# Kernel tuning notes

Measured on AMD Instinct MI355X. Metric: run time of the kernel, lower is better.

Reference implementation:

```python
import jax, jax.numpy as jnp
import numpy as np

B, NH, T, H, W = 2, 4, 8, 14, 14
DIM = 384
HD = DIM // NH  # 96 = head_dim = depthwise conv channels
N = T * H * W  # 1568 tokens, no cls
EPS = 1e-6


def _dwconv3d(x, w):
    # x: [BN, C, T, H, W], w: [C, 1, 3, 3, 3]; depthwise conv, stride 1, pad 1
    return jax.lax.conv_general_dilated(
        x, w, window_strides=(1, 1, 1), padding=[(1, 1)] * 3,
        feature_group_count=x.shape[1],
        dimension_numbers=('NCDHW', 'OIDHW', 'NCDHW'))


def _layernorm(x, g, b):
    m = jnp.mean(x, axis=-1, keepdims=True)
    v = jnp.var(x, axis=-1, keepdims=True)
    return (x - m) * jax.lax.rsqrt(v + EPS) * g + b


def _attention_pool(x4, conv_w, ln_g, ln_b, t, h, w):
    # x4: [B, nh, L, c] with L = t*h*w (no cls token)
    Bq, n, L, c = x4.shape
    y = x4.reshape(Bq * n, t, h, w, c).transpose(0, 4, 1, 2, 3)  # [(b nh), c, t, h, w]
    y = _dwconv3d(y, conv_w)
    y = y.transpose(0, 2, 3, 4, 1).reshape(Bq, n, L, c)
    return _layernorm(y, ln_g, ln_b)


def setup_inputs() -> dict:
    key = jax.random.key(0)
    ks = jax.random.split(key, 12)
    inp = {
        'x': jax.random.normal(ks[0], (B, N, DIM), jnp.float32),
        'qkv_w': jax.random.normal(ks[1], (3 * DIM, DIM), jnp.float32) * 0.02,
        'proj_w': jax.random.normal(ks[2], (DIM, DIM), jnp.float32) * 0.02,
        'proj_b': jnp.zeros((DIM,), jnp.float32),
        'pool_q_w': jax.random.normal(ks[3], (HD, 1, 3, 3, 3), jnp.float32) * 0.1,
        'pool_k_w': jax.random.normal(ks[4], (HD, 1, 3, 3, 3), jnp.float32) * 0.1,
        'pool_v_w': jax.random.normal(ks[5], (HD, 1, 3, 3, 3), jnp.float32) * 0.1,
        'norm_q_w': jnp.ones((HD,), jnp.float32), 'norm_q_b': jnp.zeros((HD,), jnp.float32),
        'norm_k_w': jnp.ones((HD,), jnp.float32), 'norm_k_b': jnp.zeros((HD,), jnp.float32),
        'norm_v_w': jnp.ones((HD,), jnp.float32), 'norm_v_b': jnp.zeros((HD,), jnp.float32),
        'rel_pos_h': jax.random.normal(ks[6], (2 * H - 1, HD), jnp.float32) * 0.02,
        'rel_pos_w': jax.random.normal(ks[7], (2 * W - 1, HD), jnp.float32) * 0.02,
        'rel_pos_t': jax.random.normal(ks[8], (2 * T - 1, HD), jnp.float32) * 0.02,
        't': T, 'h': H, 'w': W,
    }
    return inp


def reference(x, qkv_w, proj_w, proj_b, pool_q_w, pool_k_w, pool_v_w,
              norm_q_w, norm_q_b, norm_k_w, norm_k_b, norm_v_w, norm_v_b,
              rel_pos_h, rel_pos_w, rel_pos_t, t, h, w):
    Bq, Nq, _ = x.shape
    # fused QKV projection (qkv_bias=False)
    qkv = (x @ qkv_w.T).reshape(Bq, Nq, 3, NH, HD).transpose(2, 0, 3, 1, 4)
    q, k, v = qkv[0], qkv[1], qkv[2]  # [B, nh, N, hd]
    # pooled Q/K/V: depthwise conv3d + LayerNorm (stride 1 -> shapes preserved)
    q = _attention_pool(q, pool_q_w, norm_q_w, norm_q_b, t, h, w)
    k = _attention_pool(k, pool_k_w, norm_k_w, norm_k_b, t, h, w)
    v = _attention_pool(v, pool_v_w, norm_v_w, norm_v_b, t, h, w)

    scale = HD ** -0.5
    attn = jnp.einsum('bnqc,bnkc->bnqk', q * scale, k)  # [B, nh, N, N]

    # decomposed relative position biases (q_shape == k_shape, ratios == 1)
    dist_h = jnp.arange(h)[:, None] - jnp.arange(h)[None, :] + (h - 1)
    dist_w = jnp.arange(w)[:, None] - jnp.arange(w)[None, :] + (w - 1)
    dist_t = jnp.arange(t)[:, None] - jnp.arange(t)[None, :] + (t - 1)
    Rh = rel_pos_h[dist_h]  # [h, h, c]
    Rw = rel_pos_w[dist_w]  # [w, w, c]
    Rt = rel_pos_t[dist_t]  # [t, t, c]

    r_q = q.reshape(Bq, NH, t, h, w, HD)
    rel_h = jnp.einsum('bnthwc,hkc->bnthwk', r_q, Rh)  # [B,nh,t,h,w,kh]
    rel_w = jnp.einsum('bnthwc,wkc->bnthwk', r_q, Rw)  # [B,nh,t,h,w,kw]
    rel_t = jnp.einsum('bnthwc,tkc->bnthwk', r_q, Rt)  # [B,nh,t,h,w,kt]

    attn8 = attn.reshape(Bq, NH, t, h, w, t, h, w)
    attn8 = (attn8
             + rel_h[:, :, :, :, :, None, :, None]
             + rel_w[:, :, :, :, :, None, None, :]
             + rel_t[:, :, :, :, :, :, None, None])
    attn = jax.nn.softmax(attn8.reshape(Bq, NH, Nq, Nq), axis=-1)

    out = jnp.einsum('bnqk,bnkc->bnqc', attn, v)
    out = out + q  # residual pooling
    out = out.transpose(0, 2, 1, 3).reshape(Bq, Nq, DIM)
    out = out @ proj_w.T + proj_b
    return out
```

## Files before the change

kernel.cpp:

```cpp
#include <hip/hip_runtime.h>

#define B_    2
#define NH_   4
#define T_    8
#define H_    14
#define W_    14
#define HW_   196
#define HD_   96
#define DIM_  384
#define N_    1568
#define BH_   (B_*NH_)
#define BN_   (B_*N_)
#define BHN_  (BH_*N_)
#define CAUG_ 160

typedef unsigned short bf_t;
typedef unsigned int   u32;
typedef __attribute__((ext_vector_type(8))) short bf16x8;
typedef __attribute__((ext_vector_type(4))) float f32x4;

#define LOG2E 1.4426950408889634f
#define QSCALE_LOG2E 0.14724445f

static __device__ __forceinline__ float lo16(u32 v){ union{u32 i; float f;}x; x.i = v<<16;           return x.f; }
static __device__ __forceinline__ float hi16(u32 v){ union{u32 i; float f;}x; x.i = v & 0xffff0000u; return x.f; }
static __device__ __forceinline__ float b2f(bf_t v){ union{u32 i; float f;}x; x.i = ((u32)v)<<16;    return x.f; }
static __device__ __forceinline__ bf_t  f2b(float f){
  union{float f; u32 i;} x; x.f = f;
  return (bf_t)((x.i + 0x7fffu + ((x.i>>16)&1u)) >> 16);
}
static __device__ __forceinline__ u32 pack2(float a, float b){
  return (u32)f2b(a) | ((u32)f2b(b) << 16);
}
static __device__ __forceinline__ size_t ftidx(int row, int k){
  return ((((size_t)(row>>4))*12 + (k>>5))*64 + ((k>>3)&3)*16 + (row&15))*8 + (k&7);
}

#define NA_ (BN_*DIM_)
#define NB_ (3*DIM_*DIM_)
#define NC_ (DIM_*DIM_)
#define CAST_BLOCKS ((NA_+NB_+NC_)/4/256)

__global__ __launch_bounds__(256) void k_cast(
    const float* __restrict__ a, bf_t* __restrict__ ad,
    const float* __restrict__ b, bf_t* __restrict__ bd,
    const float* __restrict__ c, bf_t* __restrict__ cd,
    const float* __restrict__ wq, const float* __restrict__ wk,
    const float* __restrict__ wv, float* __restrict__ tq,
    float* __restrict__ tk, float* __restrict__ tv){
  if (blockIdx.x < CAST_BLOCKS){
    const int i = blockIdx.x*256 + threadIdx.x;
    const int i4 = i*4;
    float4 v; bf_t* dst; int row, k;
    if (i4 < NA_){
      v = ((const float4*)a)[i];
      dst = ad; row = i4/DIM_; k = i4%DIM_;
    } else if (i4 < NA_+NB_){
      const int f = i4 - NA_;
      v = ((const float4*)b)[i - NA_/4];
      dst = bd; row = f/DIM_; k = f%DIM_;
    } else {
      const int f = i4 - NA_ - NB_;
      v = ((const float4*)c)[i - (NA_+NB_)/4];
      dst = cd; row = f/DIM_; k = f%DIM_;
    }
    ushort4 o; o.x = f2b(v.x); o.y = f2b(v.y); o.z = f2b(v.z); o.w = f2b(v.w);
    *(ushort4*)(dst + ftidx(row, k)) = o;
  } else {
    const int idx = (blockIdx.x - CAST_BLOCKS)*256 + threadIdx.x;
    if (idx >= 3*HD_*27) return;
    const int t = idx / (HD_*27), rem = idx % (HD_*27);
    const int ch = rem / 27, j = rem % 27;
    const float* s = (t==0)? wq : (t==1)? wk : wv;
    float* d       = (t==0)? tq : (t==1)? tk : tv;
    d[j*HD_ + ch] = s[ch*27 + j];
  }
}

__global__ __launch_bounds__(256) void k_qkv(const bf_t* __restrict__ Xt,
    const bf_t* __restrict__ Wt,
    bf_t* __restrict__ q, bf_t* __restrict__ k, bf_t* __restrict__ v){
  const int wid = threadIdx.x >> 6, lane = threadIdx.x & 63;
  const int wr = wid & 1, wc = wid >> 1;
  const int nl = lane & 15, quad = lane >> 4;
  const int r0 = blockIdx.x*64 + wr*32;
  const int mt0 = r0 >> 4;
  const int nt0 = blockIdx.y*8 + wc*4;
  f32x4 acc[2][4];
  #pragma unroll
  for (int i = 0; i < 2; ++i)
    #pragma unroll
    for (int j = 0; j < 4; ++j) acc[i][j] = (f32x4){0.f,0.f,0.f,0.f};
  const bf_t* A0 = Xt + ((size_t)mt0*12*64 + lane)*8;
  const bf_t* B0 = Wt + ((size_t)nt0*12*64 + lane)*8;
  #pragma unroll 2
  for (int k0 = 0; k0 < 12; ++k0){
    const bf16x8 a0 = *(const bf16x8*)(A0 + k0*512);
    const bf16x8 a1 = *(const bf16x8*)(A0 + 12*512 + k0*512);
    bf16x8 bf[4];
    #pragma unroll
    for (int j = 0; j < 4; ++j) bf[j] = *(const bf16x8*)(B0 + (size_t)(j*12 + k0)*512);
    #pragma unroll
    for (int j = 0; j < 4; ++j){
      acc[0][j] = __builtin_amdgcn_mfma_f32_16x16x32_bf16(a0, bf[j], acc[0][j], 0, 0, 0);
      acc[1][j] = __builtin_amdgcn_mfma_f32_16x16x32_bf16(a1, bf[j], acc[1][j], 0, 0, 0);
    }
  }
  #pragma unroll
  for (int i = 0; i < 2; ++i){
    #pragma unroll
    for (int r = 0; r < 4; ++r){
      const int m  = r0 + i*16 + quad*4 + r;
      const int bb = m / N_, nn = m % N_;
      #pragma unroll
      for (int j = 0; j < 4; ++j){
        const int col = (nt0 + j)*16 + nl;
        const int s = col / DIM_, rem = col - s*DIM_;
        const int head = rem / HD_, hc = rem % HD_;
        bf_t* dst = (s==0) ? q : (s==1) ? k : v;
        dst[((size_t)(bb*NH_ + head)*N_ + nn)*HD_ + hc] = f2b(acc[i][j][r]);
      }
    }
  }
}

static __device__ __forceinline__ void ln_butterfly(
    float v0, float v1, float& mean, float& rstd){
  float s  = v0 + v1;
  float s2 = v0*v0 + v1*v1;
  #pragma unroll
  for (int off = 32; off > 0; off >>= 1){
    s  += __shfl_xor(s,  off);
    s2 += __shfl_xor(s2, off);
  }
  mean = s * (1.f/HD_);
  const float var = fmaxf(s2*(1.f/HD_) - mean*mean, 0.f);
  rstd = rsqrtf(var + 1e-6f);
}

__global__ __launch_bounds__(256) void k_pool_slab(
    const bf_t* __restrict__ qr_, const bf_t* __restrict__ kr_, const bf_t* __restrict__ vr_,
    const float* __restrict__ wtq, const float* __restrict__ wtk, const float* __restrict__ wtv,
    const float* __restrict__ gq, const float* __restrict__ bq,
    const float* __restrict__ gk, const float* __restrict__ bk,
    const float* __restrict__ gv, const float* __restrict__ bv,
    const float* __restrict__ rph, const float* __restrict__ rpw,
    const float* __restrict__ rpt,
    bf_t* __restrict__ qp, bf_t* __restrict__ Qaug,
    bf_t* __restrict__ Kt, bf_t* __restrict__ Vtt){
  __shared__ __align__(16) bf_t slab[162][HD_];
  __shared__ float qtmp[4][4][HD_];
  __shared__ u32 vres[16][48];
  const int wid = threadIdx.x >> 6, lane = threadIdx.x & 63;
  const int sec = blockIdx.x / 784;
  const int rr_ = blockIdx.x % 784;
  const int bh = rr_ / 98, tok0 = (rr_ % 98)*16;
  const bf_t*  src = (sec==0)? qr_ : (sec==1)? kr_ : vr_;
  const float* wt  = (sec==0)? wtq : (sec==1)? wtk : wtv;
  const float* g   = (sec==0)? gq  : (sec==1)? gk  : gv;
  const float* be  = (sec==0)? bq  : (sec==1)? bk  : bv;
  const bf_t* base = src + (size_t)bh*N_*HD_;

  for (int li = threadIdx.x; li < 162*12; li += 256){
    const int rw = li / 12, ss = li % 12;
    const int aa = rw/54, bb2 = (rw%54)/18, cc = rw%18;
    int nn = tok0 + (aa-1)*HW_ + (bb2-1)*W_ + (cc-1);
    nn = min(max(nn, 0), N_-1);
    *(uint4*)&slab[rw][ss*8] = *(const uint4*)(base + (size_t)nn*HD_ + ss*8);
  }
  __syncthreads();

  const int c0 = (lane < 48) ? 2*lane : 0;
  float2 wgt[27];
  #pragma unroll
  for (int j = 0; j < 27; ++j) wgt[j] = *(const float2*)(wt + j*HD_ + c0);
  const float gg0 = g[c0], gg1 = g[c0+1], be0 = be[c0], be1 = be[c0+1];

  #pragma unroll 1
  for (int tk = 0; tk < 4; ++tk){
    const int u = wid*4 + tk;
    const int n = tok0 + u;
    const int tt = n / HW_; const int rm = n % HW_;
    const int hh = rm / W_, ww = rm % W_;
    float v0 = 0.f, v1 = 0.f;
    #pragma unroll
    for (int j = 0; j < 27; ++j){
      const int dt = j/9 - 1, dh = (j%9)/3 - 1, dw = j%3 - 1;
      const bool ok = ((unsigned)(tt+dt) < (unsigned)T_)
                   && ((unsigned)(hh+dh) < (unsigned)H_)
                   && ((unsigned)(ww+dw) < (unsigned)W_);
      const int rj = (dt+1)*54 + (dh+1)*18 + (dw + u + 1);
      u32 d = *(const u32*)&slab[rj][c0];
      d = ok ? d : 0u;
      v0 = fmaf(wgt[j].x, lo16(d), v0);
      v1 = fmaf(wgt[j].y, hi16(d), v1);
    }
    if (lane >= 48){ v0 = 0.f; v1 = 0.f; }
    float mean, rstd;
    ln_butterfly(v0, v1, mean, rstd);
    const float y0 = (v0 - mean)*rstd*gg0 + be0;
    const float y1 = (v1 - mean)*rstd*gg1 + be1;

    if (sec == 0){
      const int token = bh*N_ + n;
      if (lane < 48){
        ((u32*)qp)  [(size_t)token*48 + lane] = pack2(y0, y1);
        ((u32*)Qaug)[(size_t)token*80 + lane] = pack2(y0*QSCALE_LOG2E, y1*QSCALE_LOG2E);
        qtmp[wid][tk][c0] = y0; qtmp[wid][tk][c0+1] = y1;
      }
      __syncthreads();
      if (lane < 36){
        const float* tb; int idx;
        if (lane < 14)      { tb = rph; idx = hh - lane      + 13; }
        else if (lane < 28) { tb = rpw; idx = ww - (lane-14) + 13; }
        else                { tb = rpt; idx = tt - (lane-28) +  7; }
        const float4* t4 = (const float4*)(tb + (size_t)idx*HD_);
        float acc = 0.f;
        #pragma unroll
        for (int i = 0; i < 24; ++i){
          const float4 rv = t4[i];
          acc += qtmp[wid][tk][4*i]*rv.x + qtmp[wid][tk][4*i+1]*rv.y
               + qtmp[wid][tk][4*i+2]*rv.z + qtmp[wid][tk][4*i+3]*rv.w;
        }
        Qaug[(size_t)token*CAUG_ + HD_ + lane] = f2b(acc * LOG2E);
      } else if (lane < 64){
        Qaug[(size_t)token*CAUG_ + HD_ + lane] = 0;
      }
    } else if (sec == 1){
      const int tl = n >> 4, nr = n & 15;
      if (lane < 48){
        const size_t idx = ((((size_t)bh*98 + tl)*5 + (lane>>4))*64
                           + ((lane&15)>>2)*16 + nr)*4 + (lane&3);
        ((u32*)Kt)[idx] = pack2(y0, y1);
      } else {
        const int m = lane - 48;
        u32 pr_[2];
        #pragma unroll
        for (int h2 = 0; h2 < 2; ++h2){
          u32 w_ = 0;
          #pragma unroll
          for (int e = 0; e < 2; ++e){
            const int jj = 4*m + 2*h2 + e;
            bool on = (jj < 14) ? (jj == hh) : (jj < 28) ? (jj-14 == ww)
                     : (jj < 36) ? (jj-28 == tt) : false;
            if (on) w_ |= (0x3F80u << (16*e));
          }
          pr_[h2] = w_;
        }
        const size_t bidx = ((((size_t)bh*98 + tl)*5 + (3 + (m>>3)))*64
                            + ((m&7)>>1)*16 + nr)*4 + 2*(m&1);
        *(uint2*)((u32*)Kt + bidx) = make_uint2(pr_[0], pr_[1]);
      }
    } else {
      if (lane < 48) vres[u][lane] = pack2(y0, y1);
    }
  }

  if (sec == 2){
    __syncthreads();
    if (threadIdx.x < 2*HD_){
      const int grp = threadIdx.x / HD_, c = threadIdx.x % HD_;
      const int t0g = grp*8;
      u32 o[4];
      #pragma unroll
      for (int i = 0; i < 4; ++i){
        const u32 a = vres[t0g + 2*i][c>>1], b = vres[t0g + 2*i+1][c>>1];
        const u32 ra = (c&1) ? (a >> 16) : (a & 0xffffu);
        const u32 rb = (c&1) ? (b >> 16) : (b & 0xffffu);
        o[i] = ra | (rb << 16);
      }
      const int n0g = tok0 + t0g;
      const int pr = n0g >> 5, qd = (n0g & 31) >> 3;
      bf_t* dst = Vtt + ((((size_t)bh*49 + pr)*6 + (c>>4))*64 + qd*16 + (c&15))*8;
      *(uint4*)dst = make_uint4(o[0], o[1], o[2], o[3]);
    }
  }
}

__global__ __launch_bounds__(512) void k_attn(
    const bf_t* __restrict__ Qaug, const bf_t* __restrict__ Kt,
    const bf_t* __restrict__ Vtt, const bf_t* __restrict__ qp,
    bf_t* __restrict__ attb){
  __shared__ __align__(16) short Pb[8][16][40];
  __shared__ bf_t Os[8][16][96];
  __shared__ float ms[8][16], ls[8][16];
  const int wid = threadIdx.x >> 6, lane = threadIdx.x & 63;
  const int bh = blockIdx.x / 98, qt = blockIdx.x % 98;
  const int q0 = qt*16;
  const int nl = lane & 15, quad = lane >> 4;

  bf16x8 qa[5];
  {
    const bf_t* Qrow = Qaug + ((size_t)bh*N_ + q0 + nl)*CAUG_ + quad*8;
    #pragma unroll
    for (int i = 0; i < 5; ++i) qa[i] = *(const bf16x8*)(Qrow + i*32);
  }
  short* Pw = &Pb[wid][0][0];

  f32x4 O[6];
  #pragma unroll
  for (int i = 0; i < 6; ++i) O[i] = (f32x4){0.f,0.f,0.f,0.f};
  float mc[4]   = {0.f,0.f,0.f,0.f};
  float rmax[4] = {-3e38f,-3e38f,-3e38f,-3e38f};
  float l[4]    = {0.f,0.f,0.f,0.f};

  auto s_tile = [&](int tl, int half){
    const bf_t* Kp = Kt + (((size_t)bh*98 + tl)*5*64 + lane)*8;
    f32x4 s = (f32x4){0.f,0.f,0.f,0.f};
    #pragma unroll
    for (int i = 0; i < 5; ++i)
      s = __builtin_amdgcn_mfma_f32_16x16x32_bf16(qa[i], *(const bf16x8*)(Kp + i*512), s, 0, 0, 0);
    #pragma unroll
    for (int r = 0; r < 4; ++r){
      rmax[r] = fmaxf(rmax[r], s[r]);
      const float p = exp2f(s[r] - mc[r]);
      l[r] += p;
      Pw[(quad*4 + r)*40 + half*16 + nl] = (short)f2b(p);
    }
  };
  auto rescale = [&](){
    #pragma unroll
    for (int r = 0; r < 4; ++r){
      float tm = rmax[r];
      tm = fmaxf(tm, __shfl_xor(tm, 1));
      tm = fmaxf(tm, __shfl_xor(tm, 2));
      tm = fmaxf(tm, __shfl_xor(tm, 4));
      tm = fmaxf(tm, __shfl_xor(tm, 8));
      const float mn = fmaxf(mc[r], tm);
      const float al = exp2f(mc[r] - mn);
      mc[r] = mn; l[r] *= al;
      #pragma unroll
      for (int ct = 0; ct < 6; ++ct) O[ct][r] *= al;
    }
  };

  const int p0 = (wid == 0) ? 0 : (7 + 6*(wid-1));
  const int npairs = (wid == 0) ? 7 : 6;
  #pragma unroll 1
  for (int pi = 0; pi < npairs; ++pi){
    const int kp = p0 + pi;
    s_tile(2*kp,     0);
    s_tile(2*kp + 1, 1);
    const bf16x8 pa = *(const bf16x8*)(Pw + nl*40 + quad*8);
    const bf_t* Vp = Vtt + (((size_t)bh*49 + kp)*6*64 + lane)*8;
    #pragma unroll
    for (int ct = 0; ct < 6; ++ct)
      O[ct] = __builtin_amdgcn_mfma_f32_16x16x32_bf16(pa, *(const bf16x8*)(Vp + ct*512), O[ct], 0, 0, 0);
    if (pi == npairs-1) rescale();
  }

  #pragma unroll
  for (int r = 0; r < 4; ++r){
    float ls_ = l[r];
    ls_ += __shfl_xor(ls_, 1); ls_ += __shfl_xor(ls_, 2);
    ls_ += __shfl_xor(ls_, 4); ls_ += __shfl_xor(ls_, 8);
    if (nl == 0){ ms[wid][quad*4 + r] = mc[r]; ls[wid][quad*4 + r] = ls_; }
    #pragma unroll
    for (int ct = 0; ct < 6; ++ct) Os[wid][quad*4 + r][ct*16 + nl] = f2b(O[ct][r]);
  }
  __syncthreads();

  const int bb = bh >> 2, head = bh & 3;
  const int grow0 = bb*N_ + q0;
  for (int e = threadIdx.x; e < 16*96; e += 512){
    const int row = e / 96, col = e % 96;
    float mx = -3e38f;
    #pragma unroll
    for (int w = 0; w < 8; ++w) mx = fmaxf(mx, ms[w][row]);
    float L = 0.f, A = 0.f;
    #pragma unroll
    for (int w = 0; w < 8; ++w){
      const float wt = exp2f(ms[w][row] - mx);
      L += wt*ls[w][row];
      A += wt*b2f(Os[w][row][col]);
    }
    const float val = A/L + b2f(qp[((size_t)bh*N_ + q0 + row)*HD_ + col]);
    attb[ftidx(grow0 + row, head*HD_ + col)] = f2b(val);
  }
}

__global__ __launch_bounds__(256) void k_proj(const bf_t* __restrict__ At,
    const bf_t* __restrict__ Wpt, const float* __restrict__ pb,
    float* __restrict__ out){
  const int wid = threadIdx.x >> 6, lane = threadIdx.x & 63;
  const int wr = wid & 1, wc = wid >> 1;
  const int nl = lane & 15, quad = lane >> 4;
  const int r0 = blockIdx.x*64 + wr*32;
  const int mt0 = r0 >> 4;
  const int nt0 = blockIdx.y*8 + wc*4;
  f32x4 acc[2][4];
  #pragma unroll
  for (int i = 0; i < 2; ++i)
    #pragma unroll
    for (int j = 0; j < 4; ++j) acc[i][j] = (f32x4){0.f,0.f,0.f,0.f};
  const bf_t* A0 = At  + ((size_t)mt0*12*64 + lane)*8;
  const bf_t* B0 = Wpt + ((size_t)nt0*12*64 + lane)*8;
  #pragma unroll 2
  for (int k0 = 0; k0 < 12; ++k0){
    const bf16x8 a0 = *(const bf16x8*)(A0 + k0*512);
    const bf16x8 a1 = *(const bf16x8*)(A0 + 12*512 + k0*512);
    bf16x8 bf[4];
    #pragma unroll
    for (int j = 0; j < 4; ++j) bf[j] = *(const bf16x8*)(B0 + (size_t)(j*12 + k0)*512);
    #pragma unroll
    for (int j = 0; j < 4; ++j){
      acc[0][j] = __builtin_amdgcn_mfma_f32_16x16x32_bf16(a0, bf[j], acc[0][j], 0, 0, 0);
      acc[1][j] = __builtin_amdgcn_mfma_f32_16x16x32_bf16(a1, bf[j], acc[1][j], 0, 0, 0);
    }
  }
  #pragma unroll
  for (int i = 0; i < 2; ++i){
    #pragma unroll
    for (int r = 0; r < 4; ++r){
      const int m = r0 + i*16 + quad*4 + r;
      #pragma unroll
      for (int j = 0; j < 4; ++j){
        const int col = (nt0 + j)*16 + nl;
        out[(size_t)m*DIM_ + col] = acc[i][j][r] + pb[col];
      }
    }
  }
}

extern "C" void kernel_launch(void* const* d_in, const int* in_sizes, int n_in,
                              void* d_out, int out_size, void* d_ws, size_t ws_size,
                              hipStream_t stream){
  const float* x      = (const float*)d_in[0];
  const float* qkv_w  = (const float*)d_in[1];
  const float* proj_w = (const float*)d_in[2];
  const float* proj_b = (const float*)d_in[3];
  const float* pqw    = (const float*)d_in[4];
  const float* pkw    = (const float*)d_in[5];
  const float* pvw    = (const float*)d_in[6];
  const float* nqw    = (const float*)d_in[7];
  const float* nqb    = (const float*)d_in[8];
  const float* nkw    = (const float*)d_in[9];
  const float* nkb    = (const float*)d_in[10];
  const float* nvw    = (const float*)d_in[11];
  const float* nvb    = (const float*)d_in[12];
  const float* rph    = (const float*)d_in[13];
  const float* rpw    = (const float*)d_in[14];
  const float* rpt    = (const float*)d_in[15];

  char* p = (char*)d_ws;
  const size_t RAW = (size_t)BH_*N_*HD_*2;
  const size_t AUG = (size_t)BH_*N_*CAUG_*2;
  bf_t* xb     = (bf_t*)(p);
  bf_t* wqkvb  = (bf_t*)(p + RAW);
  bf_t* wprojb = (bf_t*)(p + RAW + 884736);
  char* p2 = p + RAW + 884736 + 294912;
  bf_t* raw_q  = (bf_t*)(p2);
  bf_t* raw_k  = (bf_t*)(p2 + RAW);
  bf_t* raw_v  = (bf_t*)(p2 + 2*RAW);
  bf_t* attb   = raw_q;
  bf_t* qp     = (bf_t*)(p2 + 3*RAW);
  bf_t* Qaug   = (bf_t*)(p2 + 4*RAW);
  bf_t* Kt     = (bf_t*)(p2 + 4*RAW + AUG);
  bf_t* Vtt    = (bf_t*)(p2 + 4*RAW + 2*AUG);
  float* wtq   = (float*)(p2 + 4*RAW + 2*AUG + RAW);
  float* wtk   = wtq + 27*HD_;
  float* wtv   = wtk + 27*HD_;

  k_cast     <<<CAST_BLOCKS + 31, 256, 0, stream>>>(x, xb, qkv_w, wqkvb, proj_w, wprojb,
                                                    pqw, pkw, pvw, wtq, wtk, wtv);
  k_qkv      <<<dim3(BN_/64, 9),  256, 0, stream>>>(xb, wqkvb, raw_q, raw_k, raw_v);
  k_pool_slab<<<3*784,            256, 0, stream>>>(raw_q, raw_k, raw_v,
                                                    wtq, wtk, wtv,
                                                    nqw, nqb, nkw, nkb, nvw, nvb,
                                                    rph, rpw, rpt,
                                                    qp, Qaug, Kt, Vtt);
  k_attn     <<<BH_*98,           512, 0, stream>>>(Qaug, Kt, Vtt, qp, attb);
  k_proj     <<<dim3(BN_/64, 3),  256, 0, stream>>>(attb, wprojb, proj_b, (float*)d_out);
}
```

Baseline: 202.5 us.

## Reuse slab rows across four tokens and alias pool kernel shared memory

The depthwise conv in the pool kernel now loads six consecutive slab rows per (dt,dh) offset and reuses them across the four tokens each wave handles. Before, each token re-read its own 27 neighbours. Shared buffers for slab, qtmp and vres are merged into a union to cut LDS footprint, and the launch bounds request 5 blocks per CU for higher occupancy. The weight loads are hoisted ahead of the slab fill so they overlap it. Barriers are added to protect the aliased storage, and register pressure rises because four accumulators are live at once.

```diff
diff --git a/kernel.cpp b/kernel.cpp
--- a/kernel.cpp
+++ b/kernel.cpp
@@ -138,7 +138,13 @@
   rstd = rsqrtf(var + 1e-6f);
 }
 
-__global__ __launch_bounds__(256) void k_pool_slab(
+union PoolSM {
+  bf_t  slab[162][HD_];
+  float qtmp[4][4][HD_];
+  u32   vres[16][48];
+};
+
+__global__ __launch_bounds__(256, 5) void k_pool_slab(
     const bf_t* __restrict__ qr_, const bf_t* __restrict__ kr_, const bf_t* __restrict__ vr_,
     const float* __restrict__ wtq, const float* __restrict__ wtk, const float* __restrict__ wtv,
     const float* __restrict__ gq, const float* __restrict__ bq,
@@ -148,9 +154,7 @@
     const float* __restrict__ rpt,
     bf_t* __restrict__ qp, bf_t* __restrict__ Qaug,
     bf_t* __restrict__ Kt, bf_t* __restrict__ Vtt){
-  __shared__ __align__(16) bf_t slab[162][HD_];
-  __shared__ float qtmp[4][4][HD_];
-  __shared__ u32 vres[16][48];
+  __shared__ __align__(16) PoolSM sm;
   const int wid = threadIdx.x >> 6, lane = threadIdx.x & 63;
   const int sec = blockIdx.x / 784;
   const int rr_ = blockIdx.x % 784;
@@ -161,77 +165,106 @@
   const float* be  = (sec==0)? bq  : (sec==1)? bk  : bv;
   const bf_t* base = src + (size_t)bh*N_*HD_;
 
+  const int c0 = (lane < 48) ? 2*lane : 0;
+  float2 wgt[27];
+  #pragma unroll
+  for (int j = 0; j < 27; ++j) wgt[j] = *(const float2*)(wt + j*HD_ + c0);
+  const float gg0 = g[c0], gg1 = g[c0+1], be0 = be[c0], be1 = be[c0+1];
+
   for (int li = threadIdx.x; li < 162*12; li += 256){
     const int rw = li / 12, ss = li % 12;
     const int aa = rw/54, bb2 = (rw%54)/18, cc = rw%18;
     int nn = tok0 + (aa-1)*HW_ + (bb2-1)*W_ + (cc-1);
     nn = min(max(nn, 0), N_-1);
-    *(uint4*)&slab[rw][ss*8] = *(const uint4*)(base + (size_t)nn*HD_ + ss*8);
+    *(uint4*)&sm.slab[rw][ss*8] = *(const uint4*)(base + (size_t)nn*HD_ + ss*8);
   }
   __syncthreads();
 
-  const int c0 = (lane < 48) ? 2*lane : 0;
-  float2 wgt[27];
-  #pragma unroll
-  for (int j = 0; j < 27; ++j) wgt[j] = *(const float2*)(wt + j*HD_ + c0);
-  const float gg0 = g[c0], gg1 = g[c0+1], be0 = be[c0], be1 = be[c0+1];
-
-  #pragma unroll 1
+  int tt[4], hh[4], ww[4];
+  #pragma unroll
   for (int tk = 0; tk < 4; ++tk){
-    const int u = wid*4 + tk;
-    const int n = tok0 + u;
-    const int tt = n / HW_; const int rm = n % HW_;
-    const int hh = rm / W_, ww = rm % W_;
-    float v0 = 0.f, v1 = 0.f;
-    #pragma unroll
-    for (int j = 0; j < 27; ++j){
-      const int dt = j/9 - 1, dh = (j%9)/3 - 1, dw = j%3 - 1;
-      const bool ok = ((unsigned)(tt+dt) < (unsigned)T_)
-                   && ((unsigned)(hh+dh) < (unsigned)H_)
-                   && ((unsigned)(ww+dw) < (unsigned)W_);
-      const int rj = (dt+1)*54 + (dh+1)*18 + (dw + u + 1);
-      u32 d = *(const u32*)&slab[rj][c0];
-      d = ok ? d : 0u;
-      v0 = fmaf(wgt[j].x, lo16(d), v0);
-      v1 = fmaf(wgt[j].y, hi16(d), v1);
-    }
-    if (lane >= 48){ v0 = 0.f; v1 = 0.f; }
+    const int n = tok0 + wid*4 + tk;
+    tt[tk] = n / HW_;
+    const int rm = n % HW_;
+    hh[tk] = rm / W_; ww[tk] = rm % W_;
+  }
+
+  float v0[4] = {0.f,0.f,0.f,0.f}, v1[4] = {0.f,0.f,0.f,0.f};
+  #pragma unroll
+  for (int j9 = 0; j9 < 9; ++j9){
+    const int dt = j9/3 - 1, dh = j9%3 - 1;
+    const int rbase = (dt+1)*54 + (dh+1)*18 + wid*4;
+    u32 rr[6];
+    #pragma unroll
+    for (int s = 0; s < 6; ++s) rr[s] = *(const u32*)&sm.slab[rbase + s][c0];
+    #pragma unroll
+    for (int tk = 0; tk < 4; ++tk){
+      const bool okth = ((unsigned)(tt[tk]+dt) < (unsigned)T_)
+                     && ((unsigned)(hh[tk]+dh) < (unsigned)H_);
+      #pragma unroll
+      for (int dw = 0; dw < 3; ++dw){
+        const bool ok = okth && ((unsigned)(ww[tk]+dw-1) < (unsigned)W_);
+        const u32 d = ok ? rr[tk+dw] : 0u;
+        const float2 wj = wgt[j9*3 + dw];
+        v0[tk] = fmaf(wj.x, lo16(d), v0[tk]);
+        v1[tk] = fmaf(wj.y, hi16(d), v1[tk]);
+      }
+    }
+  }
+  #pragma unroll
+  for (int tk = 0; tk < 4; ++tk){
+    float a = v0[tk], b = v1[tk];
+    if (lane >= 48){ a = 0.f; b = 0.f; }
     float mean, rstd;
-    ln_butterfly(v0, v1, mean, rstd);
-    const float y0 = (v0 - mean)*rstd*gg0 + be0;
-    const float y1 = (v1 - mean)*rstd*gg1 + be1;
-
-    if (sec == 0){
+    ln_butterfly(a, b, mean, rstd);
+    v0[tk] = (a - mean)*rstd*gg0 + be0;
+    v1[tk] = (b - mean)*rstd*gg1 + be1;
+  }
+
+  if (sec == 0){
+    __syncthreads();
+    #pragma unroll
+    for (int tk = 0; tk < 4; ++tk){
+      const int n = tok0 + wid*4 + tk;
       const int token = bh*N_ + n;
       if (lane < 48){
-        ((u32*)qp)  [(size_t)token*48 + lane] = pack2(y0, y1);
-        ((u32*)Qaug)[(size_t)token*80 + lane] = pack2(y0*QSCALE_LOG2E, y1*QSCALE_LOG2E);
-        qtmp[wid][tk][c0] = y0; qtmp[wid][tk][c0+1] = y1;
-      }
-      __syncthreads();
+        ((u32*)qp)  [(size_t)token*48 + lane] = pack2(v0[tk], v1[tk]);
+        ((u32*)Qaug)[(size_t)token*80 + lane] = pack2(v0[tk]*QSCALE_LOG2E, v1[tk]*QSCALE_LOG2E);
+        *(float2*)&sm.qtmp[wid][tk][c0] = make_float2(v0[tk], v1[tk]);
+      }
+    }
+    #pragma unroll
+    for (int tk = 0; tk < 4; ++tk){
+      const int n = tok0 + wid*4 + tk;
+      const int token = bh*N_ + n;
       if (lane < 36){
         const float* tb; int idx;
-        if (lane < 14)      { tb = rph; idx = hh - lane      + 13; }
-        else if (lane < 28) { tb = rpw; idx = ww - (lane-14) + 13; }
-        else                { tb = rpt; idx = tt - (lane-28) +  7; }
+        if (lane < 14)      { tb = rph; idx = hh[tk] - lane      + 13; }
+        else if (lane < 28) { tb = rpw; idx = ww[tk] - (lane-14) + 13; }
+        else                { tb = rpt; idx = tt[tk] - (lane-28) +  7; }
         const float4* t4 = (const float4*)(tb + (size_t)idx*HD_);
+        const float4* q4 = (const float4*)&sm.qtmp[wid][tk][0];
         float acc = 0.f;
         #pragma unroll
         for (int i = 0; i < 24; ++i){
           const float4 rv = t4[i];
-          acc += qtmp[wid][tk][4*i]*rv.x + qtmp[wid][tk][4*i+1]*rv.y
-               + qtmp[wid][tk][4*i+2]*rv.z + qtmp[wid][tk][4*i+3]*rv.w;
+          const float4 qv = q4[i];
+          acc += qv.x*rv.x + qv.y*rv.y + qv.z*rv.z + qv.w*rv.w;
         }
         Qaug[(size_t)token*CAUG_ + HD_ + lane] = f2b(acc * LOG2E);
-      } else if (lane < 64){
+      } else {
         Qaug[(size_t)token*CAUG_ + HD_ + lane] = 0;
       }
-    } else if (sec == 1){
+    }
+  } else if (sec == 1){
+    #pragma unroll
+    for (int tk = 0; tk < 4; ++tk){
+      const int n = tok0 + wid*4 + tk;
       const int tl = n >> 4, nr = n & 15;
       if (lane < 48){
         const size_t idx = ((((size_t)bh*98 + tl)*5 + (lane>>4))*64
                            + ((lane&15)>>2)*16 + nr)*4 + (lane&3);
-        ((u32*)Kt)[idx] = pack2(y0, y1);
+        ((u32*)Kt)[idx] = pack2(v0[tk], v1[tk]);
       } else {
         const int m = lane - 48;
         u32 pr_[2];
@@ -241,8 +274,8 @@
           #pragma unroll
           for (int e = 0; e < 2; ++e){
             const int jj = 4*m + 2*h2 + e;
-            bool on = (jj < 14) ? (jj == hh) : (jj < 28) ? (jj-14 == ww)
-                     : (jj < 36) ? (jj-28 == tt) : false;
+            bool on = (jj < 14) ? (jj == hh[tk]) : (jj < 28) ? (jj-14 == ww[tk])
+                     : (jj < 36) ? (jj-28 == tt[tk]) : false;
             if (on) w_ |= (0x3F80u << (16*e));
           }
           pr_[h2] = w_;
@@ -251,12 +284,13 @@
                             + ((m&7)>>1)*16 + nr)*4 + 2*(m&1);
         *(uint2*)((u32*)Kt + bidx) = make_uint2(pr_[0], pr_[1]);
       }
-    } else {
-      if (lane < 48) vres[u][lane] = pack2(y0, y1);
-    }
-  }
-
-  if (sec == 2){
+    }
+  } else {
+    __syncthreads();
+    #pragma unroll
+    for (int tk = 0; tk < 4; ++tk){
+      if (lane < 48) sm.vres[wid*4 + tk][lane] = pack2(v0[tk], v1[tk]);
+    }
     __syncthreads();
     if (threadIdx.x < 2*HD_){
       const int grp = threadIdx.x / HD_, c = threadIdx.x % HD_;
@@ -264,7 +298,7 @@
       u32 o[4];
       #pragma unroll
       for (int i = 0; i < 4; ++i){
-        const u32 a = vres[t0g + 2*i][c>>1], b = vres[t0g + 2*i+1][c>>1];
+        const u32 a = sm.vres[t0g + 2*i][c>>1], b = sm.vres[t0g + 2*i+1][c>>1];
         const u32 ra = (c&1) ? (a >> 16) : (a & 0xffffu);
         const u32 rb = (c&1) ? (b >> 16) : (b & 0xffffu);
         o[i] = ra | (rb << 16);
```

Result: slower. 221.9 us (+9.6%).
